# Performance work log

Hardware: AMD Instinct MI355X
Metric: run time of the kernel (lower is better)

Reference implementation:

```python
import jax, jax.numpy as jnp
import numpy as np
import math

B, S, T, F_IN, D = 4, 4096, 4096, 127, 64

def setup_inputs() -> dict:
    key = jax.random.key(0)
    k1, k2, k3, k4 = jax.random.split(key, 4)
    return {
        "x1": jax.random.normal(k1, (B, S, F_IN), dtype=jnp.float32),
        "x2": jax.random.normal(k2, (B, T, F_IN), dtype=jnp.float32),
        "W": jax.random.normal(k3, (D, F_IN), dtype=jnp.float32) * (1.0 / math.sqrt(F_IN)),
        "b": jax.random.normal(k4, (D,), dtype=jnp.float32) * 0.01,
    }

def reference(x1, x2, W, b):
    # shared linear projection: torch Linear -> x @ W.T + b
    q = jnp.einsum('bsf,df->bsd', x1, W) + b   # [B,S,D]
    k = jnp.einsum('btf,df->btd', x2, W) + b   # [B,T,D]
    scores = jnp.einsum('bsd,btd->bst', q, k)  # [B,S,T]
    # faithful to source: v4 = v3.div(1/sqrt(D)) == v3 * sqrt(D)
    scores = scores * jnp.sqrt(jnp.float32(D))
    p = jax.nn.softmax(scores, axis=-1)        # [B,S,T]
    # dropout p=0.01 treated as eval-mode identity (deterministic reference)
    out = jnp.einsum('bst,btf->bsf', p, x2)    # [B,S,F_IN]
    return out
```

## Files before the change

### kernel.cpp

```cpp
#include <hip/hip_runtime.h>
#include <hip/hip_bf16.h>


typedef __bf16 bf16x8 __attribute__((ext_vector_type(8)));
typedef float f32x16 __attribute__((ext_vector_type(16)));

#define S_DIM 4096
#define F_DIM 127
#define QSCALE 11.5415603271f
#define THR 11.0f

static __device__ __forceinline__ unsigned cvt_pk_bf16(float lo, float hi) {
  unsigned r;
  asm("v_cvt_pk_bf16_f32 %0, %1, %2" : "=v"(r) : "v"(lo), "v"(hi));
  return r;
}
static __device__ __forceinline__ float exp2_fast(float x) {
  float r;
  asm("v_exp_f32 %0, %1" : "=v"(r) : "v"(x));
  return r;
}
static __device__ __forceinline__ bf16x8 mk_bf16x8(unsigned w0, unsigned w1,
                                                   unsigned w2, unsigned w3) {
  unsigned t[4] = {w0, w1, w2, w3};
  bf16x8 r;
  __builtin_memcpy(&r, t, 16);
  return r;
}
static __device__ __forceinline__ bf16x8 u4_bf16x8(uint4 v) {
  bf16x8 r;
  __builtin_memcpy(&r, &v, 16);
  return r;
}

__global__ __launch_bounds__(256) void wfrag_kernel(const float* __restrict__ W,
                                                    uint4* __restrict__ wf) {
  const int gid = blockIdx.x * 256 + threadIdx.x;
  const int dt = gid >> 9;
  const int kk = (gid >> 6) & 7;
  const int lane = gid & 63;
  const int d = dt * 32 + (lane & 31);
  const int f0b = kk * 16 + (lane >> 5) * 8;
  const float* wr = W + (long)d * F_DIM;
  unsigned hw[4], lw[4];
#pragma unroll
  for (int g = 0; g < 4; ++g) {
    const int f0 = f0b + 2 * g;
    const float v0 = (f0 < F_DIM) ? wr[f0] : 0.f;
    const float v1 = (f0 + 1 < F_DIM) ? wr[f0 + 1] : 0.f;
    const unsigned h = cvt_pk_bf16(v0, v1);
    const float l0 = v0 - __uint_as_float(h << 16);
    const float l1 = v1 - __uint_as_float(h & 0xffff0000u);
    hw[g] = h;
    lw[g] = cvt_pk_bf16(l0, l1);
  }
  wf[((dt * 8 + kk) * 64 + lane) * 2 + 0] = make_uint4(hw[0], hw[1], hw[2], hw[3]);
  wf[((dt * 8 + kk) * 64 + lane) * 2 + 1] = make_uint4(lw[0], lw[1], lw[2], lw[3]);
}

__global__ __launch_bounds__(256) void proj_kernel(
    const float* __restrict__ x1, const float* __restrict__ x2,
    const uint4* __restrict__ wf, const float* __restrict__ bias,
    uint4* __restrict__ qhf, uint4* __restrict__ qlf,
    uint4* __restrict__ khf, uint4* __restrict__ klf) {
  __shared__ unsigned kstage[4][32 * 66];
  const int tid = threadIdx.x;
  const int wave = tid >> 6;
  const int lane = tid & 63;
  const int arow = lane & 31;
  const int half = lane >> 5;
  const int bi = blockIdx.x;
  const bool isK = bi >= 128;
  const float* x = isK ? x2 : x1;
  const int grow0 = (bi & 127) * 128 + wave * 32;
  const float* xrow = x + (long)(grow0 + arow) * F_DIM;

  bf16x8 xh[8], xl[8];
#pragma unroll
  for (int kk = 0; kk < 8; ++kk) {
    unsigned hw[4], lw[4];
#pragma unroll
    for (int g = 0; g < 4; ++g) {
      const int f0 = kk * 16 + half * 8 + 2 * g;
      const float v0 = (f0 < F_DIM) ? xrow[f0] : 0.f;
      const float v1 = (f0 + 1 < F_DIM) ? xrow[f0 + 1] : 0.f;
      const unsigned h = cvt_pk_bf16(v0, v1);
      const float l0 = v0 - __uint_as_float(h << 16);
      const float l1 = v1 - __uint_as_float(h & 0xffff0000u);
      hw[g] = h;
      lw[g] = cvt_pk_bf16(l0, l1);
    }
    xh[kk] = mk_bf16x8(hw[0], hw[1], hw[2], hw[3]);
    xl[kk] = mk_bf16x8(lw[0], lw[1], lw[2], lw[3]);
  }

  f32x16 acc0, acc1;
#pragma unroll
  for (int r = 0; r < 16; ++r) {
    acc0[r] = 0.f;
    acc1[r] = 0.f;
  }
#pragma unroll
  for (int kk = 0; kk < 8; ++kk) {
    const bf16x8 wh0 = u4_bf16x8(wf[((0 * 8 + kk) * 64 + lane) * 2 + 0]);
    const bf16x8 wl0 = u4_bf16x8(wf[((0 * 8 + kk) * 64 + lane) * 2 + 1]);
    const bf16x8 wh1 = u4_bf16x8(wf[((1 * 8 + kk) * 64 + lane) * 2 + 0]);
    const bf16x8 wl1 = u4_bf16x8(wf[((1 * 8 + kk) * 64 + lane) * 2 + 1]);
    acc0 = __builtin_amdgcn_mfma_f32_32x32x16_bf16(xh[kk], wh0, acc0, 0, 0, 0);
    acc0 = __builtin_amdgcn_mfma_f32_32x32x16_bf16(xh[kk], wl0, acc0, 0, 0, 0);
    acc0 = __builtin_amdgcn_mfma_f32_32x32x16_bf16(xl[kk], wh0, acc0, 0, 0, 0);
    acc1 = __builtin_amdgcn_mfma_f32_32x32x16_bf16(xh[kk], wh1, acc1, 0, 0, 0);
    acc1 = __builtin_amdgcn_mfma_f32_32x32x16_bf16(xh[kk], wl1, acc1, 0, 0, 0);
    acc1 = __builtin_amdgcn_mfma_f32_32x32x16_bf16(xl[kk], wh1, acc1, 0, 0, 0);
  }

  unsigned* kst = kstage[wave];
#pragma unroll
  for (int dt = 0; dt < 2; ++dt) {
    const f32x16 acc = dt ? acc1 : acc0;
    const int d = dt * 32 + arow;
    const float bd = bias[d];
#pragma unroll
    for (int r = 0; r < 16; r += 2) {
      const int row0 = (r & 3) + 8 * (r >> 2) + 4 * half;
      float v0 = acc[r] + bd;
      float v1 = acc[r + 1] + bd;
      if (!isK) {
        v0 *= QSCALE;
        v1 *= QSCALE;
      }
      const unsigned h = cvt_pk_bf16(v0, v1);
      const float l0 = v0 - __uint_as_float(h << 16);
      const float l1 = v1 - __uint_as_float(h & 0xffff0000u);
      const unsigned l = cvt_pk_bf16(l0, l1);
      kst[row0 * 66 + d] = (h & 0xffffu) | (l << 16);
      kst[(row0 + 1) * 66 + d] = (h >> 16) | (l & 0xffff0000u);
    }
  }

  const int b = grow0 >> 12;
  const int tile = (grow0 & (S_DIM - 1)) >> 5;
  uint4* dh = (isK ? khf : qhf) + ((long)(b * 128 + tile) * 4) * 64 + lane;
  uint4* dl = (isK ? klf : qlf) + ((long)(b * 128 + tile) * 4) * 64 + lane;
#pragma unroll
  for (int kk = 0; kk < 4; ++kk) {
    const int d0 = kk * 16 + half * 8;
    unsigned w[8];
#pragma unroll
    for (int j = 0; j < 8; ++j) w[j] = kst[arow * 66 + d0 + j];
    unsigned hw[4], lw[4];
#pragma unroll
    for (int g = 0; g < 4; ++g) {
      hw[g] = (w[2 * g] & 0xffffu) | (w[2 * g + 1] << 16);
      lw[g] = (w[2 * g] >> 16) | (w[2 * g + 1] & 0xffff0000u);
    }
    dh[kk * 64] = make_uint4(hw[0], hw[1], hw[2], hw[3]);
    dl[kk * 64] = make_uint4(lw[0], lw[1], lw[2], lw[3]);
  }
}

__global__ __launch_bounds__(256) void x2repack_kernel(
    const float* __restrict__ x2, uint4* __restrict__ x2tf) {
  const int tid = threadIdx.x;
  const int bi = blockIdx.x;
  const int b = bi >> 8;
  const int tt = bi & 255;
  const int fb = tid >> 6;
  const int l = tid & 63;
  const int t0 = tt * 16 + ((l >> 5) << 3);
  const int f = fb * 32 + (l & 31);
  const float* src = x2 + ((long)b * S_DIM + t0) * F_DIM + f;
  unsigned w[4];
#pragma unroll
  for (int g = 0; g < 4; ++g) {
    const float v0 = (f < F_DIM) ? src[(long)(2 * g) * F_DIM] : 1.0f;
    const float v1 = (f < F_DIM) ? src[(long)(2 * g + 1) * F_DIM] : 1.0f;
    w[g] = cvt_pk_bf16(v0, v1);
  }
  x2tf[((long)(b * 256 + tt) * 4 + fb) * 64 + l] = make_uint4(w[0], w[1], w[2], w[3]);
}

__global__ __launch_bounds__(512, 2) void attn_kernel(
    const uint4* __restrict__ qhf, const uint4* __restrict__ qlf,
    const uint4* __restrict__ khf, const uint4* __restrict__ klf,
    const uint4* __restrict__ x2tf, float* __restrict__ out) {
  const int tid = threadIdx.x;
  const int lane = tid & 63;
  const int wave = tid >> 6;
  const int col = lane & 31;
  const int half = lane >> 5;
  const int sub = wave & 1;
  const int qtr = wave >> 1;
  const int bi = blockIdx.x;
  const int xcd = bi & 7;
  const int slot = bi >> 3;
  const int L = (xcd >> 1) * 64 + slot * 2 + (xcd & 1);
  const int b = L >> 6;
  const int q0 = (L & 63) << 6;

  const int qtile = ((q0 + sub * 32) & (S_DIM - 1)) >> 5;
  bf16x8 qh[4], ql[4];
#pragma unroll
  for (int kk = 0; kk < 4; ++kk) {
    qh[kk] = u4_bf16x8(qhf[((long)(b * 128 + qtile) * 4 + kk) * 64 + lane]);
    ql[kk] = u4_bf16x8(qlf[((long)(b * 128 + qtile) * 4 + kk) * 64 + lane]);
  }

  const uint4* khfp = khf + (long)b * 128 * 4 * 64;
  const uint4* klfp = klf + (long)b * 128 * 4 * 64;
  const uint4* xfp = x2tf + (long)b * 256 * 4 * 64;

  f32x16 a0, a1, a2, a3;
#pragma unroll
  for (int r = 0; r < 16; ++r) {
    a0[r] = 0.f; a1[r] = 0.f; a2[r] = 0.f; a3[r] = 0.f;
  }
  float m = -INFINITY;

  uint4 KA[8], KB[8];
  {
    const int t0_ = qtr;
#pragma unroll
    for (int kk = 0; kk < 4; ++kk) {
      KA[kk] = khfp[(t0_ * 4 + kk) * 64 + lane];
      KA[4 + kk] = klfp[(t0_ * 4 + kk) * 64 + lane];
    }
  }

  auto body = [&](const uint4 (&C)[8], uint4 (&N)[8], int i) {
    const int tile = (i << 2) + qtr;
    uint4 xv[8];
#pragma unroll
    for (int kf = 0; kf < 2; ++kf)
#pragma unroll
      for (int fb = 0; fb < 4; ++fb)
        xv[kf * 4 + fb] = xfp[((tile * 2 + kf) * 4 + fb) * 64 + lane];
    if (i < 31) {
      const int tn = ((i + 1) << 2) + qtr;
#pragma unroll
      for (int kk = 0; kk < 4; ++kk) {
        N[kk] = khfp[(tn * 4 + kk) * 64 + lane];
        N[4 + kk] = klfp[(tn * 4 + kk) * 64 + lane];
      }
    }
    f32x16 st;
#pragma unroll
    for (int r = 0; r < 16; ++r) st[r] = 0.f;
#pragma unroll
    for (int kk = 0; kk < 4; ++kk) {
      const bf16x8 kv = u4_bf16x8(C[kk]);
      const bf16x8 lv = u4_bf16x8(C[4 + kk]);
      st = __builtin_amdgcn_mfma_f32_32x32x16_bf16(kv, qh[kk], st, 0, 0, 0);
      st = __builtin_amdgcn_mfma_f32_32x32x16_bf16(kv, ql[kk], st, 0, 0, 0);
      st = __builtin_amdgcn_mfma_f32_32x32x16_bf16(lv, qh[kk], st, 0, 0, 0);
    }
    float pmax = st[0];
#pragma unroll
    for (int r = 1; r < 16; ++r) pmax = fmaxf(pmax, st[r]);
    pmax = fmaxf(pmax, __shfl_xor(pmax, 32));
    if (__any(pmax > m + THR)) {
      const float mnew = fmaxf(m, pmax);
      const float sc = exp2_fast(m - mnew);
#pragma unroll
      for (int r = 0; r < 16; ++r) {
        a0[r] *= sc; a1[r] *= sc; a2[r] *= sc; a3[r] *= sc;
      }
      m = mnew;
    }
    unsigned pg[4][2];
#pragma unroll
    for (int g = 0; g < 4; ++g) {
      pg[g][0] = cvt_pk_bf16(exp2_fast(st[4 * g + 0] - m),
                             exp2_fast(st[4 * g + 1] - m));
      pg[g][1] = cvt_pk_bf16(exp2_fast(st[4 * g + 2] - m),
                             exp2_fast(st[4 * g + 3] - m));
    }
#pragma unroll
    for (int kk = 0; kk < 2; ++kk) {
      unsigned x0 = pg[2 * kk][0], y0 = pg[2 * kk + 1][0];
      unsigned x1 = pg[2 * kk][1], y1 = pg[2 * kk + 1][1];
      asm("v_permlane32_swap_b32 %0, %1" : "+v"(x0), "+v"(y0));
      asm("v_permlane32_swap_b32 %0, %1" : "+v"(x1), "+v"(y1));
      const bf16x8 pf = mk_bf16x8(x0, x1, y0, y1);
      a0 = __builtin_amdgcn_mfma_f32_32x32x16_bf16(u4_bf16x8(xv[kk * 4 + 0]),
                                                   pf, a0, 0, 0, 0);
      a1 = __builtin_amdgcn_mfma_f32_32x32x16_bf16(u4_bf16x8(xv[kk * 4 + 1]),
                                                   pf, a1, 0, 0, 0);
      a2 = __builtin_amdgcn_mfma_f32_32x32x16_bf16(u4_bf16x8(xv[kk * 4 + 2]),
                                                   pf, a2, 0, 0, 0);
      a3 = __builtin_amdgcn_mfma_f32_32x32x16_bf16(u4_bf16x8(xv[kk * 4 + 3]),
                                                   pf, a3, 0, 0, 0);
    }
  };

  for (int i = 0; i < 32; i += 2) {
    body(KA, KB, i);
    body(KB, KA, i + 1);
  }

  __shared__ float mbuf[8][32];
  __shared__ float accb[2][128 * 33];
  if (lane < 32) mbuf[wave][col] = m;
  __syncthreads();
  float mstar = mbuf[sub][col];
#pragma unroll
  for (int w = 1; w < 4; ++w) mstar = fmaxf(mstar, mbuf[sub + 2 * w][col]);
  const float wsc = exp2_fast(m - mstar);
  float* buf = accb[sub];
  auto emit = [&](const f32x16& av, int fb, bool first) {
#pragma unroll
    for (int r = 0; r < 16; ++r) {
      const int f = fb * 32 + (r & 3) + 8 * (r >> 2) + 4 * half;
      const float v = av[r] * wsc;
      if (first) buf[f * 33 + col] = v;
      else buf[f * 33 + col] += v;
    }
  };
  for (int p = 0; p < 4; ++p) {
    if (qtr == p) {
      const bool first = (p == 0);
      emit(a0, 0, first);
      emit(a1, 1, first);
      emit(a2, 2, first);
      emit(a3, 3, first);
    }
    __syncthreads();
  }

  const int q64 = tid >> 3;
  const int fg = tid & 7;
  const int s2 = q64 >> 5;
  const int qq = q64 & 31;
  const float inv = 1.0f / accb[s2][127 * 33 + qq];
  float* ob = out + ((long)(b * S_DIM + q0 + q64)) * F_DIM;
#pragma unroll
  for (int j = 0; j < 16; ++j) {
    const int f = fg * 16 + j;
    if (f < F_DIM) ob[f] = accb[s2][f * 33 + qq] * inv;
  }
}

extern "C" void kernel_launch(void* const* d_in, const int* in_sizes, int n_in,
                              void* d_out, int out_size, void* d_ws,
                              size_t ws_size, hipStream_t stream) {
  const float* x1 = (const float*)d_in[0];
  const float* x2 = (const float*)d_in[1];
  const float* W = (const float*)d_in[2];
  const float* bias = (const float*)d_in[3];
  float* out = (float*)d_out;

  char* ws = (char*)d_ws;
  uint4* qhf = (uint4*)ws;
  uint4* qlf = (uint4*)(ws + (2l << 20));
  uint4* khf = (uint4*)(ws + (4l << 20));
  uint4* klf = (uint4*)(ws + (6l << 20));
  uint4* x2tf = (uint4*)(ws + (8l << 20));
  uint4* wf = (uint4*)d_out;

  hipLaunchKernelGGL(wfrag_kernel, dim3(4), dim3(256), 0, stream, W, wf);
  hipLaunchKernelGGL(proj_kernel, dim3(256), dim3(256), 0, stream, x1, x2, wf,
                     bias, qhf, qlf, khf, klf);
  hipLaunchKernelGGL(x2repack_kernel, dim3(1024), dim3(256), 0, stream, x2,
                     x2tf);
  hipLaunchKernelGGL(attn_kernel, dim3(256), dim3(512), 0, stream, qhf, qlf,
                     khf, klf, x2tf, out);
}
```

Measured before the change: 77.79 us.

## Software-pipeline QK MFMA one tile ahead of softmax and PV

```diff
diff --git a/kernel.cpp b/kernel.cpp
--- a/kernel.cpp
+++ b/kernel.cpp
@@ -19,6 +19,9 @@
   float r;
   asm("v_exp_f32 %0, %1" : "=v"(r) : "v"(x));
   return r;
+}
+static __device__ __forceinline__ float m3(float a, float b, float c) {
+  return fmaxf(fmaxf(a, b), c);
 }
 static __device__ __forceinline__ bf16x8 mk_bf16x8(unsigned w0, unsigned w1,
                                                    unsigned w2, unsigned w3) {
@@ -217,46 +220,61 @@
   }
   float m = -INFINITY;
 
-  uint4 KA[8], KB[8];
-  {
-    const int t0_ = qtr;
+  auto qk12 = [&](const uint4 (&K)[8], f32x16& st) {
+    __builtin_amdgcn_s_setprio(1);
 #pragma unroll
     for (int kk = 0; kk < 4; ++kk) {
-      KA[kk] = khfp[(t0_ * 4 + kk) * 64 + lane];
-      KA[4 + kk] = klfp[(t0_ * 4 + kk) * 64 + lane];
-    }
-  }
-
-  auto body = [&](const uint4 (&C)[8], uint4 (&N)[8], int i) {
-    const int tile = (i << 2) + qtr;
-    uint4 xv[8];
-#pragma unroll
-    for (int kf = 0; kf < 2; ++kf)
-#pragma unroll
-      for (int fb = 0; fb < 4; ++fb)
-        xv[kf * 4 + fb] = xfp[((tile * 2 + kf) * 4 + fb) * 64 + lane];
-    if (i < 31) {
-      const int tn = ((i + 1) << 2) + qtr;
-#pragma unroll
-      for (int kk = 0; kk < 4; ++kk) {
-        N[kk] = khfp[(tn * 4 + kk) * 64 + lane];
-        N[4 + kk] = klfp[(tn * 4 + kk) * 64 + lane];
-      }
-    }
-    f32x16 st;
-#pragma unroll
-    for (int r = 0; r < 16; ++r) st[r] = 0.f;
-#pragma unroll
-    for (int kk = 0; kk < 4; ++kk) {
-      const bf16x8 kv = u4_bf16x8(C[kk]);
-      const bf16x8 lv = u4_bf16x8(C[4 + kk]);
+      const bf16x8 kv = u4_bf16x8(K[kk]);
+      const bf16x8 lv = u4_bf16x8(K[4 + kk]);
       st = __builtin_amdgcn_mfma_f32_32x32x16_bf16(kv, qh[kk], st, 0, 0, 0);
       st = __builtin_amdgcn_mfma_f32_32x32x16_bf16(kv, ql[kk], st, 0, 0, 0);
       st = __builtin_amdgcn_mfma_f32_32x32x16_bf16(lv, qh[kk], st, 0, 0, 0);
     }
-    float pmax = st[0];
-#pragma unroll
-    for (int r = 1; r < 16; ++r) pmax = fmaxf(pmax, st[r]);
+    __builtin_amdgcn_s_setprio(0);
+  };
+
+  uint4 KA[8], KB[8];
+#pragma unroll
+  for (int kk = 0; kk < 4; ++kk) {
+    KA[kk] = khfp[(qtr * 4 + kk) * 64 + lane];
+    KA[4 + kk] = klfp[(qtr * 4 + kk) * 64 + lane];
+  }
+  f32x16 st0, st1;
+#pragma unroll
+  for (int r = 0; r < 16; ++r) st0[r] = 0.f;
+  qk12(KA, st0);
+  {
+    const int t1 = 4 + qtr;
+#pragma unroll
+    for (int kk = 0; kk < 4; ++kk) {
+      KB[kk] = khfp[(t1 * 4 + kk) * 64 + lane];
+      KB[4 + kk] = klfp[(t1 * 4 + kk) * 64 + lane];
+    }
+  }
+
+  auto pipe = [&](int i, f32x16& stP, f32x16& stN, uint4 (&Kq)[8],
+                  uint4 (&Kl)[8]) {
+    const int tile = (i << 2) + qtr;
+    uint4 xv[8];
+#pragma unroll
+    for (int kf = 0; kf < 2; ++kf)
+#pragma unroll
+      for (int fb = 0; fb < 4; ++fb)
+        xv[kf * 4 + fb] = xfp[((tile * 2 + kf) * 4 + fb) * 64 + lane];
+    if (i < 30) {
+      const int tn = ((i + 2) << 2) + qtr;
+#pragma unroll
+      for (int kk = 0; kk < 4; ++kk) {
+        Kl[kk] = khfp[(tn * 4 + kk) * 64 + lane];
+        Kl[4 + kk] = klfp[(tn * 4 + kk) * 64 + lane];
+      }
+    }
+    const float e0 = m3(stP[0], stP[1], stP[2]);
+    const float e1 = m3(stP[3], stP[4], stP[5]);
+    const float e2 = m3(stP[6], stP[7], stP[8]);
+    const float e3 = m3(stP[9], stP[10], stP[11]);
+    const float e4 = m3(stP[12], stP[13], stP[14]);
+    float pmax = fmaxf(m3(e0, e1, e2), m3(e3, e4, stP[15]));
     pmax = fmaxf(pmax, __shfl_xor(pmax, 32));
     if (__any(pmax > m + THR)) {
       const float mnew = fmaxf(m, pmax);
@@ -267,14 +285,20 @@
       }
       m = mnew;
     }
+    if (i < 31) {
+#pragma unroll
+      for (int r = 0; r < 16; ++r) stN[r] = 0.f;
+      qk12(Kq, stN);
+    }
     unsigned pg[4][2];
 #pragma unroll
     for (int g = 0; g < 4; ++g) {
-      pg[g][0] = cvt_pk_bf16(exp2_fast(st[4 * g + 0] - m),
-                             exp2_fast(st[4 * g + 1] - m));
-      pg[g][1] = cvt_pk_bf16(exp2_fast(st[4 * g + 2] - m),
-                             exp2_fast(st[4 * g + 3] - m));
-    }
+      pg[g][0] = cvt_pk_bf16(exp2_fast(stP[4 * g + 0] - m),
+                             exp2_fast(stP[4 * g + 1] - m));
+      pg[g][1] = cvt_pk_bf16(exp2_fast(stP[4 * g + 2] - m),
+                             exp2_fast(stP[4 * g + 3] - m));
+    }
+    __builtin_amdgcn_s_setprio(1);
 #pragma unroll
     for (int kk = 0; kk < 2; ++kk) {
       unsigned x0 = pg[2 * kk][0], y0 = pg[2 * kk + 1][0];
@@ -291,11 +315,12 @@
       a3 = __builtin_amdgcn_mfma_f32_32x32x16_bf16(u4_bf16x8(xv[kk * 4 + 3]),
                                                    pf, a3, 0, 0, 0);
     }
+    __builtin_amdgcn_s_setprio(0);
   };
 
   for (int i = 0; i < 32; i += 2) {
-    body(KA, KB, i);
-    body(KB, KA, i + 1);
+    pipe(i, st0, st1, KB, KA);
+    pipe(i + 1, st1, st0, KA, KB);
   }
 
   __shared__ float mbuf[8][32];
```

Result: slower. 99.38 us (+27.8%).

## Merge prep kernels into one launch and split score MFMA chains with priority hints

Applied to the files above, without the earlier changes.

```diff
diff --git a/kernel.cpp b/kernel.cpp
--- a/kernel.cpp
+++ b/kernel.cpp
@@ -19,6 +19,9 @@
   float r;
   asm("v_exp_f32 %0, %1" : "=v"(r) : "v"(x));
   return r;
+}
+static __device__ __forceinline__ float m3(float a, float b, float c) {
+  return fmaxf(fmaxf(a, b), c);
 }
 static __device__ __forceinline__ bf16x8 mk_bf16x8(unsigned w0, unsigned w1,
                                                    unsigned w2, unsigned w3) {
@@ -32,44 +35,67 @@
   __builtin_memcpy(&r, &v, 16);
   return r;
 }
-
-__global__ __launch_bounds__(256) void wfrag_kernel(const float* __restrict__ W,
-                                                    uint4* __restrict__ wf) {
-  const int gid = blockIdx.x * 256 + threadIdx.x;
-  const int dt = gid >> 9;
-  const int kk = (gid >> 6) & 7;
-  const int lane = gid & 63;
-  const int d = dt * 32 + (lane & 31);
-  const int f0b = kk * 16 + (lane >> 5) * 8;
-  const float* wr = W + (long)d * F_DIM;
-  unsigned hw[4], lw[4];
-#pragma unroll
-  for (int g = 0; g < 4; ++g) {
-    const int f0 = f0b + 2 * g;
-    const float v0 = (f0 < F_DIM) ? wr[f0] : 0.f;
-    const float v1 = (f0 + 1 < F_DIM) ? wr[f0 + 1] : 0.f;
-    const unsigned h = cvt_pk_bf16(v0, v1);
-    const float l0 = v0 - __uint_as_float(h << 16);
-    const float l1 = v1 - __uint_as_float(h & 0xffff0000u);
-    hw[g] = h;
-    lw[g] = cvt_pk_bf16(l0, l1);
-  }
-  wf[((dt * 8 + kk) * 64 + lane) * 2 + 0] = make_uint4(hw[0], hw[1], hw[2], hw[3]);
-  wf[((dt * 8 + kk) * 64 + lane) * 2 + 1] = make_uint4(lw[0], lw[1], lw[2], lw[3]);
-}
-
-__global__ __launch_bounds__(256) void proj_kernel(
+static __device__ __forceinline__ void split8(float4 a, float4 b, bf16x8& hv,
+                                              bf16x8& lv) {
+  const unsigned h0 = cvt_pk_bf16(a.x, a.y);
+  const unsigned h1 = cvt_pk_bf16(a.z, a.w);
+  const unsigned h2 = cvt_pk_bf16(b.x, b.y);
+  const unsigned h3 = cvt_pk_bf16(b.z, b.w);
+  const unsigned l0 = cvt_pk_bf16(a.x - __uint_as_float(h0 << 16),
+                                  a.y - __uint_as_float(h0 & 0xffff0000u));
+  const unsigned l1 = cvt_pk_bf16(a.z - __uint_as_float(h1 << 16),
+                                  a.w - __uint_as_float(h1 & 0xffff0000u));
+  const unsigned l2 = cvt_pk_bf16(b.x - __uint_as_float(h2 << 16),
+                                  b.y - __uint_as_float(h2 & 0xffff0000u));
+  const unsigned l3 = cvt_pk_bf16(b.z - __uint_as_float(h3 << 16),
+                                  b.w - __uint_as_float(h3 & 0xffff0000u));
+  hv = mk_bf16x8(h0, h1, h2, h3);
+  lv = mk_bf16x8(l0, l1, l2, l3);
+}
+
+__global__ __launch_bounds__(256) void prep_kernel(
     const float* __restrict__ x1, const float* __restrict__ x2,
-    const uint4* __restrict__ wf, const float* __restrict__ bias,
+    const float* __restrict__ W, const float* __restrict__ bias,
     uint4* __restrict__ qhf, uint4* __restrict__ qlf,
-    uint4* __restrict__ khf, uint4* __restrict__ klf) {
-  __shared__ unsigned kstage[4][32 * 66];
+    uint4* __restrict__ khf, uint4* __restrict__ klf,
+    uint4* __restrict__ x2tf) {
+  __shared__ unsigned shbuf[8448];
   const int tid = threadIdx.x;
+  const int bi = blockIdx.x;
+
+  if (bi >= 256) {
+    const int ri = bi - 256;
+    const int b = ri >> 8;
+    const int tt = ri & 255;
+    const int fb = tid >> 6;
+    const int l = tid & 63;
+    const int t0 = tt * 16 + ((l >> 5) << 3);
+    const int f = fb * 32 + (l & 31);
+    const float* src = x2 + ((long)b * S_DIM + t0) * F_DIM + f;
+    unsigned w[4];
+#pragma unroll
+    for (int g = 0; g < 4; ++g) {
+      const float v0 = (f < F_DIM) ? src[(long)(2 * g) * F_DIM] : 1.0f;
+      const float v1 = (f < F_DIM) ? src[(long)(2 * g + 1) * F_DIM] : 1.0f;
+      w[g] = cvt_pk_bf16(v0, v1);
+    }
+    x2tf[((long)(b * 256 + tt) * 4 + fb) * 64 + l] =
+        make_uint4(w[0], w[1], w[2], w[3]);
+    return;
+  }
+
+  float* shw = (float*)shbuf;
+  for (int idx = tid; idx < 64 * 128; idx += 256) {
+    const int d = idx >> 7;
+    const int f = idx & 127;
+    shw[d * 132 + f] = (f < F_DIM) ? W[d * F_DIM + f] : 0.f;
+  }
+  __syncthreads();
+
   const int wave = tid >> 6;
   const int lane = tid & 63;
   const int arow = lane & 31;
   const int half = lane >> 5;
-  const int bi = blockIdx.x;
   const bool isK = bi >= 128;
   const float* x = isK ? x2 : x1;
   const int grow0 = (bi & 127) * 128 + wave * 32;
@@ -78,20 +104,17 @@
   bf16x8 xh[8], xl[8];
 #pragma unroll
   for (int kk = 0; kk < 8; ++kk) {
-    unsigned hw[4], lw[4];
-#pragma unroll
-    for (int g = 0; g < 4; ++g) {
-      const int f0 = kk * 16 + half * 8 + 2 * g;
-      const float v0 = (f0 < F_DIM) ? xrow[f0] : 0.f;
-      const float v1 = (f0 + 1 < F_DIM) ? xrow[f0 + 1] : 0.f;
-      const unsigned h = cvt_pk_bf16(v0, v1);
-      const float l0 = v0 - __uint_as_float(h << 16);
-      const float l1 = v1 - __uint_as_float(h & 0xffff0000u);
-      hw[g] = h;
-      lw[g] = cvt_pk_bf16(l0, l1);
-    }
-    xh[kk] = mk_bf16x8(hw[0], hw[1], hw[2], hw[3]);
-    xl[kk] = mk_bf16x8(lw[0], lw[1], lw[2], lw[3]);
+    const int f0 = kk * 16 + half * 8;
+    float4 a, b;
+    a.x = (f0 + 0 < F_DIM) ? xrow[f0 + 0] : 0.f;
+    a.y = (f0 + 1 < F_DIM) ? xrow[f0 + 1] : 0.f;
+    a.z = (f0 + 2 < F_DIM) ? xrow[f0 + 2] : 0.f;
+    a.w = (f0 + 3 < F_DIM) ? xrow[f0 + 3] : 0.f;
+    b.x = (f0 + 4 < F_DIM) ? xrow[f0 + 4] : 0.f;
+    b.y = (f0 + 5 < F_DIM) ? xrow[f0 + 5] : 0.f;
+    b.z = (f0 + 6 < F_DIM) ? xrow[f0 + 6] : 0.f;
+    b.w = (f0 + 7 < F_DIM) ? xrow[f0 + 7] : 0.f;
+    split8(a, b, xh[kk], xl[kk]);
   }
 
   f32x16 acc0, acc1;
@@ -102,10 +125,18 @@
   }
 #pragma unroll
   for (int kk = 0; kk < 8; ++kk) {
-    const bf16x8 wh0 = u4_bf16x8(wf[((0 * 8 + kk) * 64 + lane) * 2 + 0]);
-    const bf16x8 wl0 = u4_bf16x8(wf[((0 * 8 + kk) * 64 + lane) * 2 + 1]);
-    const bf16x8 wh1 = u4_bf16x8(wf[((1 * 8 + kk) * 64 + lane) * 2 + 0]);
-    const bf16x8 wl1 = u4_bf16x8(wf[((1 * 8 + kk) * 64 + lane) * 2 + 1]);
+    const int f0 = kk * 16 + half * 8;
+    bf16x8 wh0, wl0, wh1, wl1;
+    {
+      const float4 a = *(const float4*)&shw[arow * 132 + f0];
+      const float4 b = *(const float4*)&shw[arow * 132 + f0 + 4];
+      split8(a, b, wh0, wl0);
+    }
+    {
+      const float4 a = *(const float4*)&shw[(32 + arow) * 132 + f0];
+      const float4 b = *(const float4*)&shw[(32 + arow) * 132 + f0 + 4];
+      split8(a, b, wh1, wl1);
+    }
     acc0 = __builtin_amdgcn_mfma_f32_32x32x16_bf16(xh[kk], wh0, acc0, 0, 0, 0);
     acc0 = __builtin_amdgcn_mfma_f32_32x32x16_bf16(xh[kk], wl0, acc0, 0, 0, 0);
     acc0 = __builtin_amdgcn_mfma_f32_32x32x16_bf16(xl[kk], wh0, acc0, 0, 0, 0);
@@ -113,8 +144,9 @@
     acc1 = __builtin_amdgcn_mfma_f32_32x32x16_bf16(xh[kk], wl1, acc1, 0, 0, 0);
     acc1 = __builtin_amdgcn_mfma_f32_32x32x16_bf16(xl[kk], wh1, acc1, 0, 0, 0);
   }
-
-  unsigned* kst = kstage[wave];
+  __syncthreads();
+
+  unsigned* kst = shbuf + wave * 2112;
 #pragma unroll
   for (int dt = 0; dt < 2; ++dt) {
     const f32x16 acc = dt ? acc1 : acc0;
@@ -157,27 +189,6 @@
     dh[kk * 64] = make_uint4(hw[0], hw[1], hw[2], hw[3]);
     dl[kk * 64] = make_uint4(lw[0], lw[1], lw[2], lw[3]);
   }
-}
-
-__global__ __launch_bounds__(256) void x2repack_kernel(
-    const float* __restrict__ x2, uint4* __restrict__ x2tf) {
-  const int tid = threadIdx.x;
-  const int bi = blockIdx.x;
-  const int b = bi >> 8;
-  const int tt = bi & 255;
-  const int fb = tid >> 6;
-  const int l = tid & 63;
-  const int t0 = tt * 16 + ((l >> 5) << 3);
-  const int f = fb * 32 + (l & 31);
-  const float* src = x2 + ((long)b * S_DIM + t0) * F_DIM + f;
-  unsigned w[4];
-#pragma unroll
-  for (int g = 0; g < 4; ++g) {
-    const float v0 = (f < F_DIM) ? src[(long)(2 * g) * F_DIM] : 1.0f;
-    const float v1 = (f < F_DIM) ? src[(long)(2 * g + 1) * F_DIM] : 1.0f;
-    w[g] = cvt_pk_bf16(v0, v1);
-  }
-  x2tf[((long)(b * 256 + tt) * 4 + fb) * 64 + l] = make_uint4(w[0], w[1], w[2], w[3]);
 }
 
 __global__ __launch_bounds__(512, 2) void attn_kernel(
@@ -218,23 +229,14 @@
   float m = -INFINITY;
 
   uint4 KA[8], KB[8];
-  {
-    const int t0_ = qtr;
-#pragma unroll
-    for (int kk = 0; kk < 4; ++kk) {
-      KA[kk] = khfp[(t0_ * 4 + kk) * 64 + lane];
-      KA[4 + kk] = klfp[(t0_ * 4 + kk) * 64 + lane];
-    }
+#pragma unroll
+  for (int kk = 0; kk < 4; ++kk) {
+    KA[kk] = khfp[(qtr * 4 + kk) * 64 + lane];
+    KA[4 + kk] = klfp[(qtr * 4 + kk) * 64 + lane];
   }
 
   auto body = [&](const uint4 (&C)[8], uint4 (&N)[8], int i) {
     const int tile = (i << 2) + qtr;
-    uint4 xv[8];
-#pragma unroll
-    for (int kf = 0; kf < 2; ++kf)
-#pragma unroll
-      for (int fb = 0; fb < 4; ++fb)
-        xv[kf * 4 + fb] = xfp[((tile * 2 + kf) * 4 + fb) * 64 + lane];
     if (i < 31) {
       const int tn = ((i + 1) << 2) + qtr;
 #pragma unroll
@@ -243,20 +245,40 @@
         N[4 + kk] = klfp[(tn * 4 + kk) * 64 + lane];
       }
     }
-    f32x16 st;
-#pragma unroll
-    for (int r = 0; r < 16; ++r) st[r] = 0.f;
+    f32x16 sa, sb;
+#pragma unroll
+    for (int r = 0; r < 16; ++r) {
+      sa[r] = 0.f;
+      sb[r] = 0.f;
+    }
+    __builtin_amdgcn_s_setprio(1);
 #pragma unroll
     for (int kk = 0; kk < 4; ++kk) {
       const bf16x8 kv = u4_bf16x8(C[kk]);
       const bf16x8 lv = u4_bf16x8(C[4 + kk]);
-      st = __builtin_amdgcn_mfma_f32_32x32x16_bf16(kv, qh[kk], st, 0, 0, 0);
-      st = __builtin_amdgcn_mfma_f32_32x32x16_bf16(kv, ql[kk], st, 0, 0, 0);
-      st = __builtin_amdgcn_mfma_f32_32x32x16_bf16(lv, qh[kk], st, 0, 0, 0);
-    }
-    float pmax = st[0];
-#pragma unroll
-    for (int r = 1; r < 16; ++r) pmax = fmaxf(pmax, st[r]);
+      sa = __builtin_amdgcn_mfma_f32_32x32x16_bf16(kv, qh[kk], sa, 0, 0, 0);
+      sb = __builtin_amdgcn_mfma_f32_32x32x16_bf16(kv, ql[kk], sb, 0, 0, 0);
+      if (kk < 2)
+        sa = __builtin_amdgcn_mfma_f32_32x32x16_bf16(lv, qh[kk], sa, 0, 0, 0);
+      else
+        sb = __builtin_amdgcn_mfma_f32_32x32x16_bf16(lv, qh[kk], sb, 0, 0, 0);
+    }
+    __builtin_amdgcn_s_setprio(0);
+    uint4 xv[8];
+#pragma unroll
+    for (int kf = 0; kf < 2; ++kf)
+#pragma unroll
+      for (int fb = 0; fb < 4; ++fb)
+        xv[kf * 4 + fb] = xfp[((tile * 2 + kf) * 4 + fb) * 64 + lane];
+    f32x16 st;
+#pragma unroll
+    for (int r = 0; r < 16; ++r) st[r] = sa[r] + sb[r];
+    const float e0 = m3(st[0], st[1], st[2]);
+    const float e1 = m3(st[3], st[4], st[5]);
+    const float e2 = m3(st[6], st[7], st[8]);
+    const float e3 = m3(st[9], st[10], st[11]);
+    const float e4 = m3(st[12], st[13], st[14]);
+    float pmax = fmaxf(m3(e0, e1, e2), m3(e3, e4, st[15]));
     pmax = fmaxf(pmax, __shfl_xor(pmax, 32));
     if (__any(pmax > m + THR)) {
       const float mnew = fmaxf(m, pmax);
@@ -275,6 +297,7 @@
       pg[g][1] = cvt_pk_bf16(exp2_fast(st[4 * g + 2] - m),
                              exp2_fast(st[4 * g + 3] - m));
     }
+    __builtin_amdgcn_s_setprio(1);
 #pragma unroll
     for (int kk = 0; kk < 2; ++kk) {
       unsigned x0 = pg[2 * kk][0], y0 = pg[2 * kk + 1][0];
@@ -291,6 +314,7 @@
       a3 = __builtin_amdgcn_mfma_f32_32x32x16_bf16(u4_bf16x8(xv[kk * 4 + 3]),
                                                    pf, a3, 0, 0, 0);
     }
+    __builtin_amdgcn_s_setprio(0);
   };
 
   for (int i = 0; i < 32; i += 2) {
@@ -355,13 +379,9 @@
   uint4* khf = (uint4*)(ws + (4l << 20));
   uint4* klf = (uint4*)(ws + (6l << 20));
   uint4* x2tf = (uint4*)(ws + (8l << 20));
-  uint4* wf = (uint4*)d_out;
-
-  hipLaunchKernelGGL(wfrag_kernel, dim3(4), dim3(256), 0, stream, W, wf);
-  hipLaunchKernelGGL(proj_kernel, dim3(256), dim3(256), 0, stream, x1, x2, wf,
-                     bias, qhf, qlf, khf, klf);
-  hipLaunchKernelGGL(x2repack_kernel, dim3(1024), dim3(256), 0, stream, x2,
-                     x2tf);
+
+  hipLaunchKernelGGL(prep_kernel, dim3(1280), dim3(256), 0, stream, x1, x2, W,
+                     bias, qhf, qlf, khf, klf, x2tf);
   hipLaunchKernelGGL(attn_kernel, dim3(256), dim3(512), 0, stream, qhf, qlf,
                      khf, klf, x2tf, out);
 }
```

New measurement: 86.99 us. 11.8% more time.
